# Kernel optimization log

Hardware: AMD Instinct MI355X
Metric: run time of the kernel (lower is better)

Reference implementation:

```python
import jax, jax.numpy as jnp
import numpy as np
import math

B, S, D = 4, 2048, 1024
TAU = 0.5

def setup_inputs() -> dict:
    key = jax.random.key(0)
    ks = jax.random.split(key, 10)
    s = 1.0 / math.sqrt(D)
    return {
        "node_emb": jax.random.normal(ks[0], (B, S, D), jnp.float32),
        "label_emb": jax.random.normal(ks[1], (B, S, D), jnp.float32),
        "Wq": jax.random.uniform(ks[2], (D, D), jnp.float32, -s, s),
        "bq": jax.random.uniform(ks[3], (D,), jnp.float32, -s, s),
        "Wk": jax.random.uniform(ks[4], (D, D), jnp.float32, -s, s),
        "bk": jax.random.uniform(ks[5], (D,), jnp.float32, -s, s),
        "Wv": jax.random.uniform(ks[6], (D, D), jnp.float32, -s, s),
        "bv": jax.random.uniform(ks[7], (D,), jnp.float32, -s, s),
        "Wp": jax.random.uniform(ks[8], (D, D), jnp.float32, -s, s),
        "bp": jax.random.uniform(ks[9], (D,), jnp.float32, -s, s),
    }

def reference(node_emb, label_emb, Wq, bq, Wk, bk, Wv, bv, Wp, bp):
    # Q from label_emb; K, V from node_emb (torch Linear: x @ W.T + b)
    Q = label_emb @ Wq.T + bq          # [B, S, D]
    K = node_emb @ Wk.T + bk           # [B, S, D]
    V = node_emb @ Wv.T + bv           # [B, S, D]
    d = node_emb.shape[-1]
    score = jnp.einsum('bqd,bkd->bqk', Q, K) / jnp.sqrt(jnp.float32(d))
    # causal (lower-triangular) mask, masked_fill(-1e9) BEFORE the tau scale
    causal = jnp.tril(jnp.ones((score.shape[-2], score.shape[-1]), bool))
    score = jnp.where(causal[None, :, :], score, jnp.float32(-1e9))
    attn = jax.nn.softmax(score * TAU, axis=-1)  # [B, S, S]
    # proj_drop is Dropout(0.1); reference runs in eval mode (identity)
    z = jnp.einsum('bqk,bkd->bqd', attn, V)
    return z @ Wp.T + bp
```

## Files before the change

kernel.cpp:

```cpp
#include <hip/hip_runtime.h>
#include <hip/hip_bf16.h>
#include <stdint.h>

using bf16 = __hip_bfloat16;
typedef __bf16 bf16x8 __attribute__((ext_vector_type(8)));
typedef float f32x4 __attribute__((ext_vector_type(4)));
typedef unsigned short u16x8 __attribute__((ext_vector_type(8)));
typedef unsigned short u16x4 __attribute__((ext_vector_type(4)));

#define AS1 __attribute__((address_space(1)))
#define AS3 __attribute__((address_space(3)))

__device__ inline unsigned short f2b(float f) {
    union { __hip_bfloat16 h; unsigned short u; } cv;
    cv.h = __float2bfloat16(f);
    return cv.u;
}

__global__ __launch_bounds__(256) void cvt_pair(const float* __restrict__ a, const float* __restrict__ b,
                                                u16x8* __restrict__ oa, u16x8* __restrict__ ob, long n8) {
    const float* in = blockIdx.y ? b : a;
    u16x8* out = blockIdx.y ? ob : oa;
    long i = (long)blockIdx.x * blockDim.x + threadIdx.x;
    const long stride = (long)gridDim.x * blockDim.x;
    const float4* in4 = (const float4*)in;
    for (; i < n8; i += stride) {
        float4 x = in4[2 * i], y = in4[2 * i + 1];
        u16x8 o;
        o[0] = f2b(x.x); o[1] = f2b(x.y); o[2] = f2b(x.z); o[3] = f2b(x.w);
        o[4] = f2b(y.x); o[5] = f2b(y.y); o[6] = f2b(y.z); o[7] = f2b(y.w);
        out[i] = o;
    }
}

__global__ __launch_bounds__(256) void cvt_quad(const float* __restrict__ a, const float* __restrict__ b,
                                                const float* __restrict__ c, const float* __restrict__ d,
                                                u16x8* __restrict__ oa, u16x8* __restrict__ ob,
                                                u16x8* __restrict__ oc, u16x8* __restrict__ od, long n8) {
    const int y = blockIdx.y;
    const float* in = y == 0 ? a : (y == 1 ? b : (y == 2 ? c : d));
    u16x8* out = y == 0 ? oa : (y == 1 ? ob : (y == 2 ? oc : od));
    long i = (long)blockIdx.x * blockDim.x + threadIdx.x;
    const long stride = (long)gridDim.x * blockDim.x;
    const float4* in4 = (const float4*)in;
    for (; i < n8; i += stride) {
        float4 x = in4[2 * i], z = in4[2 * i + 1];
        u16x8 o;
        o[0] = f2b(x.x); o[1] = f2b(x.y); o[2] = f2b(x.z); o[3] = f2b(x.w);
        o[4] = f2b(z.x); o[5] = f2b(z.y); o[6] = f2b(z.z); o[7] = f2b(z.w);
        out[i] = o;
    }
}

template <typename T> __device__ inline void storev(T* p, float v);
template <> __device__ inline void storev<float>(float* p, float v) { *p = v; }
template <> __device__ inline void storev<bf16>(bf16* p, float v) { *p = __float2bfloat16(v); }

template <typename OutT, int MODE, int BN>
__global__ __launch_bounds__(512, 2) void gemmX(
    const bf16* __restrict__ A0, const bf16* __restrict__ A1,
    const bf16* __restrict__ B0p, const bf16* __restrict__ B1p,
    OutT* __restrict__ C0, OutT* __restrict__ C1,
    const float* __restrict__ bias0, const float* __restrict__ bias1,
    float scale, int lda, int ldb, int ldc, int Kdim,
    long sA, long sB, long sC)
{
    constexpr int LDSZ = (BN == 256) ? 131072 : 98304;
    constexpr int BUFS = (BN == 256) ? 65536 : 49152;
    __shared__ __align__(16) char lds[LDSZ];

    const int nwg = gridDim.x;
    const int bid = blockIdx.x;
    const int s = (nwg & 7) ? bid : ((bid & 7) * (nwg >> 3) + (bid >> 3));

    int bm, ccol0, rowB0, seg = 0;
    const bf16 *A, *B;
    OutT* C;
    const float* bias = nullptr;

    if constexpr (MODE == 0) {
        bm = s >> 3; const int bnl = s & 7; seg = bnl >> 2;
        A = A0; B = B0p; rowB0 = bnl * 256;
        C = seg ? C1 : C0; bias = seg ? bias1 : bias0;
        ccol0 = (bnl & 3) * 256;
    } else if constexpr (MODE == 1) {
        seg = s >> 7; const int r = s & 127; bm = r >> 2; const int bn = r & 3;
        A = seg ? A1 : A0; B = seg ? B1p : B0p;
        C = seg ? C1 : C0; bias = seg ? nullptr : bias0;
        rowB0 = bn * 256; ccol0 = bn * 256;
    } else if constexpr (MODE == 2) {
        const int z = s / 36, f = s % 36;
        int m = 0;
        while ((m + 1) * (m + 2) / 2 <= f) ++m;
        bm = m; const int bn = f - m * (m + 1) / 2;
        A = A0 + (long)z * sA; B = B0p + (long)z * sB; C = C0 + (long)z * sC;
        rowB0 = bn * 256; ccol0 = bn * 256;
    } else {
        const int z = s >> 6, r = s & 63; bm = r >> 3; const int bn = r & 7;
        A = A0 + (long)z * sA; B = B0p + (long)z * sB; C = C0 + (long)z * sC;
        rowB0 = bn * 128; ccol0 = bn * 128; bias = bias0;
    }

    int KT = Kdim >> 6;
    if constexpr (MODE == 3) { const int lim = 4 * (bm + 1); if (lim < KT) KT = lim; }
    const int NIT = KT >> 1;

    const int tid = threadIdx.x;
    const int lane = tid & 63;
    const int w = tid >> 6;
    constexpr int WR = (BN == 256) ? 128 : 64;
    const int wm = (BN == 256) ? (w >> 2) : (w >> 1);
    const int wn = (BN == 256) ? (w & 3) : (w & 1);

    const int rowA0 = bm * 256;

    const int rr  = tid >> 3;
    const int lch = (tid & 7) ^ (rr & 7);
    const bf16* gAt = A + (long)(rowA0 + rr) * lda + lch * 8;
    const bf16* gBt = B + (long)(rowB0 + rr) * ldb + lch * 8;

#define LA(b) (lds + (b) * BUFS)
#define LB(b) (lds + 32768 + (b) * BUFS)

    auto SG2 = [&](const bf16* g, int ld, char* dst) {
        __builtin_amdgcn_global_load_lds((const AS1 void*)g,
            (AS3 void*)(dst + tid * 16), 16, 0, 0);
        __builtin_amdgcn_global_load_lds((const AS1 void*)(g + (long)64 * ld),
            (AS3 void*)(dst + 8192 + tid * 16), 16, 0, 0);
    };
    auto ST_A = [&](int kt, int half, int b) {
        SG2(gAt + (long)kt * 64 + (long)half * 128 * lda, lda, LA(b) + half * 16384);
    };
    auto ST_B = [&](int kt, int half, int b) {
        SG2(gBt + (long)kt * 64 + (long)half * 128 * ldb, ldb, LB(b) + half * 16384);
    };
    auto ST_B1 = [&](int kt, int b) {
        SG2(gBt + (long)kt * 64, ldb, LB(b));
    };

    const int abase = (wm * WR + (lane & 15)) * 128;
    const int bbase = (wn * 64 + (lane & 15)) * 128;
    const int cc0 = (((lane >> 4) << 4)) ^ ((lane & 7) << 4);
    const int cc1 = cc0 ^ 64;

#define RAF(b, mh, mi, kk) (*(const bf16x8*)(LA(b) + abase + (mh)*8192 + (mi)*2048 + ((kk) ? cc1 : cc0)))
#define RBF(b, ni, kk)     (*(const bf16x8*)(LB(b) + bbase + (ni)*2048 + ((kk) ? cc1 : cc0)))

    f32x4 acc[(BN == 256) ? 8 : 4][4] = {};
    bf16x8 ar[4][2], blo[2][2], bhi[2][2];

#define RD_A2(b, mh, MI0) { ar[MI0][0] = RAF(b, mh, MI0, 0); ar[MI0][1] = RAF(b, mh, MI0, 1); \
                            ar[(MI0)+1][0] = RAF(b, mh, (MI0)+1, 0); ar[(MI0)+1][1] = RAF(b, mh, (MI0)+1, 1); }
#define RD_BLO(b)   { blo[0][0] = RBF(b, 0, 0); blo[0][1] = RBF(b, 0, 1); blo[1][0] = RBF(b, 1, 0); blo[1][1] = RBF(b, 1, 1); }
#define RD_BHI(b)   { bhi[0][0] = RBF(b, 2, 0); bhi[0][1] = RBF(b, 2, 1); bhi[1][0] = RBF(b, 3, 0); bhi[1][1] = RBF(b, 3, 1); }

#define MQ1(MI, bb, MH, NB) { \
    f32x4 t0_ = acc[(MH)*4 + (MI)][(NB)]; \
    t0_ = __builtin_amdgcn_mfma_f32_16x16x32_bf16(ar[MI][0], bb[0][0], t0_, 0, 0, 0); \
    t0_ = __builtin_amdgcn_mfma_f32_16x16x32_bf16(ar[MI][1], bb[0][1], t0_, 0, 0, 0); \
    acc[(MH)*4 + (MI)][(NB)] = t0_; \
    f32x4 t1_ = acc[(MH)*4 + (MI)][(NB) + 1]; \
    t1_ = __builtin_amdgcn_mfma_f32_16x16x32_bf16(ar[MI][0], bb[1][0], t1_, 0, 0, 0); \
    t1_ = __builtin_amdgcn_mfma_f32_16x16x32_bf16(ar[MI][1], bb[1][1], t1_, 0, 0, 0); \
    acc[(MH)*4 + (MI)][(NB) + 1] = t1_; }

#define WAIT_LGKM0 { asm volatile("s_waitcnt lgkmcnt(0)" ::: "memory"); __builtin_amdgcn_sched_barrier(0); }
#define WAIT_LGKM4 { asm volatile("s_waitcnt lgkmcnt(4)" ::: "memory"); __builtin_amdgcn_sched_barrier(0); }
#define SCHEDB     __builtin_amdgcn_sched_barrier(0)
#define PRE_SYNC { asm volatile("s_waitcnt lgkmcnt(0)" ::: "memory"); __builtin_amdgcn_sched_barrier(0); \
                   __builtin_amdgcn_s_barrier(); __builtin_amdgcn_sched_barrier(0); }

    auto BAR = [&]() { __builtin_amdgcn_s_barrier(); SCHEDB; };
    auto PRIO1 = [&]() { __builtin_amdgcn_s_setprio(1); };
    auto PRIO0 = [&]() { __builtin_amdgcn_s_setprio(0); };

    if constexpr (BN == 256) {
        ST_A(0, 0, 0); ST_A(0, 1, 0); ST_B(0, 0, 0); ST_B(0, 1, 0);
        ST_B(1, 0, 1); ST_B(1, 1, 1);
        asm volatile("s_waitcnt vmcnt(4)" ::: "memory");
        BAR();
        RD_BLO(0); RD_A2(0, 0, 0); RD_A2(0, 0, 2);

        for (int i = 0; i < NIT; ++i) {
            const int t0 = 2 * i;
            const bool last = (i == NIT - 1);

            ST_A(t0 + 1, 0, 1);
            PRE_SYNC; PRIO1();
            RD_BHI(0);
            MQ1(0, blo, 0, 0); MQ1(1, blo, 0, 0); MQ1(2, blo, 0, 0); MQ1(3, blo, 0, 0);
            PRIO0();

            ST_A(t0 + 1, 1, 1);
            PRE_SYNC; PRIO1();
            MQ1(0, bhi, 0, 2); MQ1(1, bhi, 0, 2); MQ1(2, bhi, 0, 2); MQ1(3, bhi, 0, 2);
            RD_A2(0, 1, 0); RD_A2(0, 1, 2);
            PRIO0();

            if (!last) ST_B(t0 + 2, 0, 0);
            PRE_SYNC; PRIO1();
            MQ1(0, bhi, 1, 2); MQ1(1, bhi, 1, 2); MQ1(2, bhi, 1, 2); MQ1(3, bhi, 1, 2);
            PRIO0();

            if (!last) { ST_B(t0 + 2, 1, 0);
                         asm volatile("s_waitcnt vmcnt(4)" ::: "memory"); }
            else       { asm volatile("s_waitcnt vmcnt(0)" ::: "memory"); }
            PRE_SYNC; PRIO1();
            MQ1(0, blo, 1, 0); MQ1(1, blo, 1, 0); MQ1(2, blo, 1, 0); MQ1(3, blo, 1, 0);
            RD_BLO(1); RD_A2(1, 0, 0); RD_A2(1, 0, 2);
            PRIO0();

            if (!last) ST_A(t0 + 2, 0, 0);
            PRE_SYNC; PRIO1();
            RD_BHI(1);
            MQ1(0, blo, 0, 0); MQ1(1, blo, 0, 0); MQ1(2, blo, 0, 0); MQ1(3, blo, 0, 0);
            PRIO0();

            if (!last) ST_A(t0 + 2, 1, 0);
            PRE_SYNC; PRIO1();
            MQ1(0, bhi, 0, 2); MQ1(1, bhi, 0, 2); MQ1(2, bhi, 0, 2); MQ1(3, bhi, 0, 2);
            RD_A2(1, 1, 0); RD_A2(1, 1, 2);
            PRIO0();

            if (!last) ST_B(t0 + 3, 0, 1);
            PRE_SYNC; PRIO1();
            MQ1(0, bhi, 1, 2); MQ1(1, bhi, 1, 2); MQ1(2, bhi, 1, 2); MQ1(3, bhi, 1, 2);
            PRIO0();

            if (!last) { ST_B(t0 + 3, 1, 1);
                         asm volatile("s_waitcnt vmcnt(4)" ::: "memory"); }
            PRE_SYNC; PRIO1();
            MQ1(0, blo, 1, 0); MQ1(1, blo, 1, 0); MQ1(2, blo, 1, 0); MQ1(3, blo, 1, 0);
            if (!last) { RD_BLO(0); RD_A2(0, 0, 0); RD_A2(0, 0, 2); }
            PRIO0();
        }
    } else {
        ST_A(0, 0, 0); ST_A(0, 1, 0); ST_B1(0, 0);
        ST_A(1, 0, 1); ST_A(1, 1, 1); ST_B1(1, 1);
        asm volatile("s_waitcnt vmcnt(6)" ::: "memory");
        BAR();

        for (int i = 0; i < NIT; ++i) {
            const int t0 = 2 * i;
            const bool last = (i == NIT - 1);

            RD_BLO(0); RD_A2(0, 0, 0); RD_A2(0, 0, 2); SCHEDB; RD_BHI(0);
            BAR(); WAIT_LGKM4; PRIO1();
            MQ1(0, blo, 0, 0); MQ1(1, blo, 0, 0); MQ1(2, blo, 0, 0); MQ1(3, blo, 0, 0);
            PRIO0(); BAR();

            if (!last) { ST_A(t0 + 2, 0, 0); ST_A(t0 + 2, 1, 0);
                         asm volatile("s_waitcnt vmcnt(4)" ::: "memory"); }
            else       { asm volatile("s_waitcnt vmcnt(0)" ::: "memory"); }
            BAR(); WAIT_LGKM0; PRIO1();
            MQ1(0, bhi, 0, 2); MQ1(1, bhi, 0, 2); MQ1(2, bhi, 0, 2); MQ1(3, bhi, 0, 2);
            PRIO0(); BAR();

            RD_BLO(1); RD_A2(1, 0, 0); RD_A2(1, 0, 2); SCHEDB; RD_BHI(1);
            if (!last) ST_B1(t0 + 2, 0);
            BAR(); WAIT_LGKM4; PRIO1();
            MQ1(0, blo, 0, 0); MQ1(1, blo, 0, 0); MQ1(2, blo, 0, 0); MQ1(3, blo, 0, 0);
            PRIO0(); BAR();

            if (!last) { ST_A(t0 + 3, 0, 1); ST_A(t0 + 3, 1, 1); ST_B1(t0 + 3, 1);
                         asm volatile("s_waitcnt vmcnt(6)" ::: "memory"); }
            BAR(); WAIT_LGKM0; PRIO1();
            MQ1(0, bhi, 0, 2); MQ1(1, bhi, 0, 2); MQ1(2, bhi, 0, 2); MQ1(3, bhi, 0, 2);
            PRIO0(); BAR();
        }
    }

    if constexpr (BN == 256) {
        char* tw = lds + w * 16384;
        if (MODE == 1 && seg == 1) {
#pragma unroll
            for (int ni = 0; ni < 4; ++ni) {
                const int cl = ni * 16 + (lane & 15);
                const int sw = 8 * (cl & 7);
#pragma unroll
                for (int mi = 0; mi < 8; ++mi) {
                    const int rlb = mi * 16 + ((lane >> 4) << 2);
                    u16x4 o;
                    o[0] = f2b(acc[mi][ni][0]); o[1] = f2b(acc[mi][ni][1]);
                    o[2] = f2b(acc[mi][ni][2]); o[3] = f2b(acc[mi][ni][3]);
                    *(u16x4*)(tw + cl * 256 + 2 * (rlb ^ sw)) = o;
                }
            }
            asm volatile("s_waitcnt lgkmcnt(0)" ::: "memory");
            __builtin_amdgcn_sched_barrier(0);
            const int m0 = rowA0 + wm * 128;
            const int z2 = m0 >> 11, mr = m0 & 2047;
            bf16* CT = (bf16*)C + (long)z2 * 2097152 + (long)(ccol0 + wn * 64 + lane) * 2048 + mr;
            const char* tr = tw + lane * 256;
            const int sw2 = lane & 7;
#pragma unroll
            for (int rb = 0; rb < 16; ++rb) {
                u16x8 v = *(const u16x8*)(tr + 16 * (rb ^ sw2));
                *(u16x8*)(CT + 8 * rb) = v;
            }
        } else {
            const int q = lane >> 4, t = lane & 15;
            const int c0 = ccol0 + wn * 64 + t;
#pragma unroll
            for (int mi = 0; mi < 8; ++mi) {
                char* tm = tw + mi * 2048;
#pragma unroll
                for (int ni = 0; ni < 4; ++ni) {
                    const float bv = bias ? bias[c0 + ni * 16] : 0.0f;
                    const int cb = (t + 16 * ni) * 2;
#pragma unroll
                    for (int j = 0; j < 4; ++j) {
                        const int rl = q * 4 + j;
                        *(bf16*)(tm + rl * 128 + (cb ^ ((rl & 7) << 4))) =
                            __float2bfloat16(acc[mi][ni][j] * scale + bv);
                    }
                }
            }
            asm volatile("s_waitcnt lgkmcnt(0)" ::: "memory");
            __builtin_amdgcn_sched_barrier(0);
            const int rr2 = lane >> 2, chb = (lane & 3) * 2;
            const int gr0 = rowA0 + wm * 128;
            bf16* Cb = (bf16*)C;
            const int gcb = ccol0 + wn * 64;
#pragma unroll
            for (int mi = 0; mi < 8; ++mi) {
                const char* tm = tw + mi * 2048;
                const long gr = gr0 + mi * 16 + rr2;
#pragma unroll
                for (int k = 0; k < 2; ++k) {
                    const int chunk = chb + k;
                    u16x8 v = *(const u16x8*)(tm + rr2 * 128 + ((chunk << 4) ^ ((rr2 & 7) << 4)));
                    *(u16x8*)(Cb + gr * (long)ldc + gcb + chunk * 8) = v;
                }
            }
        }
    } else {
        const int r0 = rowA0 + wm * WR + ((lane >> 4) << 2);
        const int c0 = ccol0 + wn * 64 + (lane & 15);
        const bool HB = (bias != nullptr);
#pragma unroll
        for (int ni = 0; ni < 4; ++ni) {
            const int c = c0 + ni * 16;
            const float bv = HB ? bias[c] : 0.0f;
#pragma unroll
            for (int mi = 0; mi < 4; ++mi) {
#pragma unroll
                for (int j = 0; j < 4; ++j) {
                    const long r = r0 + mi * 16 + j;
                    storev<OutT>(&C[r * (long)ldc + c], acc[mi][ni][j] * scale + bv);
                }
            }
        }
    }
#undef RAF
#undef RBF
#undef RD_A2
#undef RD_BLO
#undef RD_BHI
#undef MQ1
#undef LA
#undef LB
}

__global__ __launch_bounds__(256) void softmax_causal(bf16* __restrict__ SP, int S) {
    const int i = blockIdx.x;
    bf16* row = SP + ((long)blockIdx.y * S + i) * (long)S;
    const int L = i + 1;
    const int tid = threadIdx.x;
    const int lane = tid & 63, wid = tid >> 6;

    float v[8];
    int nv = 0;
    float m = -3.0e38f;
    for (int j = tid; j < L; j += 256) {
        float x = __bfloat162float(row[j]);
        v[nv++] = x;
        m = fmaxf(m, x);
    }
#pragma unroll
    for (int d = 32; d; d >>= 1) m = fmaxf(m, __shfl_xor(m, d));
    __shared__ float redm[4], reds[4];
    if (lane == 0) redm[wid] = m;
    __syncthreads();
    m = fmaxf(fmaxf(redm[0], redm[1]), fmaxf(redm[2], redm[3]));

    float ssum = 0.f;
    for (int t = 0; t < nv; ++t) { v[t] = __expf(v[t] - m); ssum += v[t]; }
#pragma unroll
    for (int d = 32; d; d >>= 1) ssum += __shfl_xor(ssum, d);
    if (lane == 0) reds[wid] = ssum;
    __syncthreads();
    ssum = reds[0] + reds[1] + reds[2] + reds[3];
    const float inv = 1.0f / ssum;

    nv = 0;
    for (int j = tid; j < L; j += 256) row[j] = __float2bfloat16(v[nv++] * inv);
    const int Lpad = ((i >> 8) + 1) << 8;
    for (int j = L + tid; j < Lpad; j += 256) row[j] = __float2bfloat16(0.0f);
}

extern "C" void kernel_launch(void* const* d_in, const int* in_sizes, int n_in,
                              void* d_out, int out_size, void* d_ws, size_t ws_size,
                              hipStream_t stream) {
    const int B = 4, S = 2048, D = 1024;
    const long MD = (long)B * S * D;
    const float scale = 0.5f / 32.0f;

    const float* node  = (const float*)d_in[0];
    const float* label = (const float*)d_in[1];
    const float* Wq = (const float*)d_in[2];
    const float* bq = (const float*)d_in[3];
    const float* Wk = (const float*)d_in[4];
    const float* bk = (const float*)d_in[5];
    const float* Wv = (const float*)d_in[6];
    const float* bv = (const float*)d_in[7];
    const float* Wp = (const float*)d_in[8];
    const float* bp = (const float*)d_in[9];
    float* out = (float*)d_out;

    char* ws = (char*)d_ws;
    bf16* nodeb  = (bf16*)(ws);
    bf16* VTb    = nodeb;
    bf16* labelb = (bf16*)(ws + 16777216);
    bf16* Wqb = (bf16*)(ws + 33554432);
    bf16* Wkb = (bf16*)(ws + 35651584);
    bf16* Wvb = (bf16*)(ws + 37748736);
    bf16* Wpb = (bf16*)(ws + 39845888);
    bf16* Qb  = (bf16*)(ws + 41943040);
    bf16* Kb  = (bf16*)(ws + 58720256);
    bf16* Vb  = (bf16*)(ws + 75497472);
    bf16* SP  = (bf16*)(ws + 92274688);
    if (ws_size < 125829120UL) return;

    dim3 blk(256);

    cvt_pair<<<dim3(512, 2), blk, 0, stream>>>(node, label, (u16x8*)nodeb, (u16x8*)labelb, MD / 8);
    cvt_quad<<<dim3(64, 4), blk, 0, stream>>>(Wq, Wk, Wv, Wp,
        (u16x8*)Wqb, (u16x8*)Wkb, (u16x8*)Wvb, (u16x8*)Wpb, (long)D * D / 8);

    gemmX<bf16, 0, 256><<<256, 512, 0, stream>>>(
        nodeb, nullptr, Wkb, nullptr, Kb, Vb, bk, bv,
        1.0f, D, D, D, D, 0, 0, 0);

    gemmX<bf16, 1, 256><<<256, 512, 0, stream>>>(
        labelb, Vb, Wqb, Wpb, Qb, VTb, bq, nullptr,
        1.0f, D, D, D, D, 0, 0, 0);

    gemmX<bf16, 2, 256><<<144, 512, 0, stream>>>(
        Qb, nullptr, Kb, nullptr, SP, nullptr, nullptr, nullptr,
        scale, D, D, S, D, (long)S * D, (long)S * D, (long)S * S);

    softmax_causal<<<dim3(S, B), blk, 0, stream>>>(SP, S);

    gemmX<float, 3, 128><<<256, 512, 0, stream>>>(
        SP, nullptr, VTb, nullptr, out, nullptr, bp, nullptr,
        1.0f, S, S, D, S, (long)S * S, (long)D * S, (long)S * D);
}
```

Baseline: 182.9 us.

## Fuse causal softmax into score GEMM epilogue and PV GEMM normalization

Removes the standalone softmax kernel. The score GEMM epilogue now applies exp and the causal mask and writes per-tile row partial sums. The PV GEMM prologue sums those partials and scales its output rows by the inverse. Max subtraction is dropped, which relies on scores being small enough not to overflow exp. The two conversion kernels are also merged into a single launch.

```diff
diff --git a/kernel.cpp b/kernel.cpp
--- a/kernel.cpp
+++ b/kernel.cpp
@@ -17,29 +17,19 @@
     return cv.u;
 }
 
-__global__ __launch_bounds__(256) void cvt_pair(const float* __restrict__ a, const float* __restrict__ b,
-                                                u16x8* __restrict__ oa, u16x8* __restrict__ ob, long n8) {
-    const float* in = blockIdx.y ? b : a;
-    u16x8* out = blockIdx.y ? ob : oa;
-    long i = (long)blockIdx.x * blockDim.x + threadIdx.x;
-    const long stride = (long)gridDim.x * blockDim.x;
-    const float4* in4 = (const float4*)in;
-    for (; i < n8; i += stride) {
-        float4 x = in4[2 * i], y = in4[2 * i + 1];
-        u16x8 o;
-        o[0] = f2b(x.x); o[1] = f2b(x.y); o[2] = f2b(x.z); o[3] = f2b(x.w);
-        o[4] = f2b(y.x); o[5] = f2b(y.y); o[6] = f2b(y.z); o[7] = f2b(y.w);
-        out[i] = o;
-    }
-}
-
-__global__ __launch_bounds__(256) void cvt_quad(const float* __restrict__ a, const float* __restrict__ b,
-                                                const float* __restrict__ c, const float* __restrict__ d,
-                                                u16x8* __restrict__ oa, u16x8* __restrict__ ob,
-                                                u16x8* __restrict__ oc, u16x8* __restrict__ od, long n8) {
+__global__ __launch_bounds__(256) void cvt6(
+    const float* __restrict__ i0, const float* __restrict__ i1,
+    const float* __restrict__ i2, const float* __restrict__ i3,
+    const float* __restrict__ i4, const float* __restrict__ i5,
+    u16x8* __restrict__ o0, u16x8* __restrict__ o1,
+    u16x8* __restrict__ o2, u16x8* __restrict__ o3,
+    u16x8* __restrict__ o4, u16x8* __restrict__ o5,
+    long nbig, long nsmall)
+{
     const int y = blockIdx.y;
-    const float* in = y == 0 ? a : (y == 1 ? b : (y == 2 ? c : d));
-    u16x8* out = y == 0 ? oa : (y == 1 ? ob : (y == 2 ? oc : od));
+    const float* in = y == 0 ? i0 : (y == 1 ? i1 : (y == 2 ? i2 : (y == 3 ? i3 : (y == 4 ? i4 : i5))));
+    u16x8* out = y == 0 ? o0 : (y == 1 ? o1 : (y == 2 ? o2 : (y == 3 ? o3 : (y == 4 ? o4 : o5))));
+    const long n8 = (y < 2) ? nbig : nsmall;
     long i = (long)blockIdx.x * blockDim.x + threadIdx.x;
     const long stride = (long)gridDim.x * blockDim.x;
     const float4* in4 = (const float4*)in;
@@ -65,7 +55,7 @@
     float scale, int lda, int ldb, int ldc, int Kdim,
     long sA, long sB, long sC)
 {
-    constexpr int LDSZ = (BN == 256) ? 131072 : 98304;
+    constexpr int LDSZ = (BN == 256) ? 131072 : ((MODE == 3) ? 99328 : 98304);
     constexpr int BUFS = (BN == 256) ? 65536 : 49152;
     __shared__ __align__(16) char lds[LDSZ];
 
@@ -73,7 +63,7 @@
     const int bid = blockIdx.x;
     const int s = (nwg & 7) ? bid : ((bid & 7) * (nwg >> 3) + (bid >> 3));
 
-    int bm, ccol0, rowB0, seg = 0;
+    int bm, ccol0, rowB0, seg = 0, bn_s = 0, zidx = 0;
     const bf16 *A, *B;
     OutT* C;
     const float* bias = nullptr;
@@ -93,10 +83,12 @@
         int m = 0;
         while ((m + 1) * (m + 2) / 2 <= f) ++m;
         bm = m; const int bn = f - m * (m + 1) / 2;
+        bn_s = bn; zidx = z;
         A = A0 + (long)z * sA; B = B0p + (long)z * sB; C = C0 + (long)z * sC;
         rowB0 = bn * 256; ccol0 = bn * 256;
     } else {
         const int z = s >> 6, r = s & 63; bm = r >> 3; const int bn = r & 7;
+        zidx = z;
         A = A0 + (long)z * sA; B = B0p + (long)z * sB; C = C0 + (long)z * sC;
         rowB0 = bn * 128; ccol0 = bn * 128; bias = bias0;
     }
@@ -113,6 +105,19 @@
     const int wn = (BN == 256) ? (w & 3) : (w & 1);
 
     const int rowA0 = bm * 256;
+
+    float* invl = (float*)(lds + 98304);
+    if constexpr (MODE == 3) {
+        if (tid < 256) {
+            const float* part = (const float*)B1p + (((long)zidx * 8 + bm) * 32) * 256 + tid;
+            float sum = 0.f;
+            const int n4 = 4 * (bm + 1);
+            for (int b4 = 0; b4 < n4; ++b4) sum += part[(long)b4 * 256];
+            invl[tid] = 1.0f / sum;
+        }
+        asm volatile("s_waitcnt lgkmcnt(0)" ::: "memory");
+        __builtin_amdgcn_sched_barrier(0);
+    }
 
     const int rr  = tid >> 3;
     const int lch = (tid & 7) ^ (rr & 7);
@@ -272,6 +277,42 @@
 
     if constexpr (BN == 256) {
         char* tw = lds + w * 16384;
+        if constexpr (MODE == 2) {
+            const int q = lane >> 4, t = lane & 15;
+            const bool diag = (bm == bn_s);
+#pragma unroll
+            for (int mi = 0; mi < 8; ++mi)
+#pragma unroll
+                for (int ni = 0; ni < 4; ++ni)
+#pragma unroll
+                    for (int j = 0; j < 4; ++j) {
+                        float e = __expf(acc[mi][ni][j] * scale);
+                        if (diag) {
+                            const int rl = wm * 128 + mi * 16 + q * 4 + j;
+                            const int cl = wn * 64 + t + ni * 16;
+                            if (cl > rl) e = 0.f;
+                        }
+                        e = __bfloat162float(__float2bfloat16(e));
+                        acc[mi][ni][j] = e;
+                    }
+            float* part = (float*)C1 + ((((long)zidx * 8 + bm) * 32) + bn_s * 4 + wn) * 256;
+#pragma unroll
+            for (int mi = 0; mi < 8; ++mi) {
+                float rs0 = acc[mi][0][0] + acc[mi][1][0] + acc[mi][2][0] + acc[mi][3][0];
+                float rs1 = acc[mi][0][1] + acc[mi][1][1] + acc[mi][2][1] + acc[mi][3][1];
+                float rs2 = acc[mi][0][2] + acc[mi][1][2] + acc[mi][2][2] + acc[mi][3][2];
+                float rs3 = acc[mi][0][3] + acc[mi][1][3] + acc[mi][2][3] + acc[mi][3][3];
+#pragma unroll
+                for (int d = 1; d < 16; d <<= 1) {
+                    rs0 += __shfl_xor(rs0, d); rs1 += __shfl_xor(rs1, d);
+                    rs2 += __shfl_xor(rs2, d); rs3 += __shfl_xor(rs3, d);
+                }
+                if (t == mi) {
+                    float4 o; o.x = rs0; o.y = rs1; o.z = rs2; o.w = rs3;
+                    *(float4*)(part + wm * 128 + mi * 16 + q * 4) = o;
+                }
+            }
+        }
         if (MODE == 1 && seg == 1) {
 #pragma unroll
             for (int ni = 0; ni < 4; ++ni) {
@@ -299,6 +340,7 @@
                 *(u16x8*)(CT + 8 * rb) = v;
             }
         } else {
+            const float sc2 = (MODE == 2) ? 1.0f : scale;
             const int q = lane >> 4, t = lane & 15;
             const int c0 = ccol0 + wn * 64 + t;
 #pragma unroll
@@ -312,7 +354,7 @@
                     for (int j = 0; j < 4; ++j) {
                         const int rl = q * 4 + j;
                         *(bf16*)(tm + rl * 128 + (cb ^ ((rl & 7) << 4))) =
-                            __float2bfloat16(acc[mi][ni][j] * scale + bv);
+                            __float2bfloat16(acc[mi][ni][j] * sc2 + bv);
                     }
                 }
             }
@@ -335,19 +377,22 @@
             }
         }
     } else {
-        const int r0 = rowA0 + wm * WR + ((lane >> 4) << 2);
+        const int q = lane >> 4;
+        const int r0 = rowA0 + wm * WR + (q << 2);
+        const int rl0 = wm * WR + (q << 2);
         const int c0 = ccol0 + wn * 64 + (lane & 15);
-        const bool HB = (bias != nullptr);
-#pragma unroll
-        for (int ni = 0; ni < 4; ++ni) {
-            const int c = c0 + ni * 16;
-            const float bv = HB ? bias[c] : 0.0f;
-#pragma unroll
-            for (int mi = 0; mi < 4; ++mi) {
-#pragma unroll
-                for (int j = 0; j < 4; ++j) {
-                    const long r = r0 + mi * 16 + j;
-                    storev<OutT>(&C[r * (long)ldc + c], acc[mi][ni][j] * scale + bv);
+#pragma unroll
+        for (int mi = 0; mi < 4; ++mi) {
+#pragma unroll
+            for (int j = 0; j < 4; ++j) {
+                const int rl = rl0 + mi * 16 + j;
+                const float iv = (MODE == 3) ? invl[rl] : scale;
+                const long r = r0 + mi * 16 + j;
+#pragma unroll
+                for (int ni = 0; ni < 4; ++ni) {
+                    const int c = c0 + ni * 16;
+                    const float bv = bias ? bias[c] : 0.0f;
+                    storev<OutT>(&C[r * (long)ldc + c], acc[mi][ni][j] * iv + bv);
                 }
             }
         }
@@ -360,43 +405,6 @@
 #undef MQ1
 #undef LA
 #undef LB
-}
-
-__global__ __launch_bounds__(256) void softmax_causal(bf16* __restrict__ SP, int S) {
-    const int i = blockIdx.x;
-    bf16* row = SP + ((long)blockIdx.y * S + i) * (long)S;
-    const int L = i + 1;
-    const int tid = threadIdx.x;
-    const int lane = tid & 63, wid = tid >> 6;
-
-    float v[8];
-    int nv = 0;
-    float m = -3.0e38f;
-    for (int j = tid; j < L; j += 256) {
-        float x = __bfloat162float(row[j]);
-        v[nv++] = x;
-        m = fmaxf(m, x);
-    }
-#pragma unroll
-    for (int d = 32; d; d >>= 1) m = fmaxf(m, __shfl_xor(m, d));
-    __shared__ float redm[4], reds[4];
-    if (lane == 0) redm[wid] = m;
-    __syncthreads();
-    m = fmaxf(fmaxf(redm[0], redm[1]), fmaxf(redm[2], redm[3]));
-
-    float ssum = 0.f;
-    for (int t = 0; t < nv; ++t) { v[t] = __expf(v[t] - m); ssum += v[t]; }
-#pragma unroll
-    for (int d = 32; d; d >>= 1) ssum += __shfl_xor(ssum, d);
-    if (lane == 0) reds[wid] = ssum;
-    __syncthreads();
-    ssum = reds[0] + reds[1] + reds[2] + reds[3];
-    const float inv = 1.0f / ssum;
-
-    nv = 0;
-    for (int j = tid; j < L; j += 256) row[j] = __float2bfloat16(v[nv++] * inv);
-    const int Lpad = ((i >> 8) + 1) << 8;
-    for (int j = L + tid; j < Lpad; j += 256) row[j] = __float2bfloat16(0.0f);
 }
 
 extern "C" void kernel_launch(void* const* d_in, const int* in_sizes, int n_in,
@@ -429,14 +437,14 @@
     bf16* Qb  = (bf16*)(ws + 41943040);
     bf16* Kb  = (bf16*)(ws + 58720256);
     bf16* Vb  = (bf16*)(ws + 75497472);
+    float* partial = (float*)(ws + 75497472);
     bf16* SP  = (bf16*)(ws + 92274688);
     if (ws_size < 125829120UL) return;
 
-    dim3 blk(256);
-
-    cvt_pair<<<dim3(512, 2), blk, 0, stream>>>(node, label, (u16x8*)nodeb, (u16x8*)labelb, MD / 8);
-    cvt_quad<<<dim3(64, 4), blk, 0, stream>>>(Wq, Wk, Wv, Wp,
-        (u16x8*)Wqb, (u16x8*)Wkb, (u16x8*)Wvb, (u16x8*)Wpb, (long)D * D / 8);
+    cvt6<<<dim3(512, 6), 256, 0, stream>>>(
+        node, label, Wq, Wk, Wv, Wp,
+        (u16x8*)nodeb, (u16x8*)labelb, (u16x8*)Wqb, (u16x8*)Wkb, (u16x8*)Wvb, (u16x8*)Wpb,
+        MD / 8, (long)D * D / 8);
 
     gemmX<bf16, 0, 256><<<256, 512, 0, stream>>>(
         nodeb, nullptr, Wkb, nullptr, Kb, Vb, bk, bv,
@@ -447,12 +455,10 @@
         1.0f, D, D, D, D, 0, 0, 0);
 
     gemmX<bf16, 2, 256><<<144, 512, 0, stream>>>(
-        Qb, nullptr, Kb, nullptr, SP, nullptr, nullptr, nullptr,
+        Qb, nullptr, Kb, nullptr, SP, (bf16*)partial, nullptr, nullptr,
         scale, D, D, S, D, (long)S * D, (long)S * D, (long)S * S);
 
-    softmax_causal<<<dim3(S, B), blk, 0, stream>>>(SP, S);
-
     gemmX<float, 3, 128><<<256, 512, 0, stream>>>(
-        SP, nullptr, VTb, nullptr, out, nullptr, bp, nullptr,
+        SP, nullptr, VTb, (const bf16*)partial, out, nullptr, bp, nullptr,
         1.0f, S, S, D, S, (long)S * S, (long)D * S, (long)S * D);
 }
```

New measurement: 172.3 us. 1.06x faster.
